# Kernel optimization log

Measured on AMD Instinct MI355X. Metric: run time of the kernel, lower is better.

The kernel has to match this reference:

```python
import jax
import jax.numpy as jnp
import numpy as np
from jax import lax

# Butterworth order-2 lowpass, Wn=0.25 (scipy.signal.butter(2, 0.25))
_B = [0.0976310729378175, 0.195262145875635, 0.0976310729378175]
_A = [1.0, -0.9428090415820634, 0.33333333333333337]


def setup_inputs() -> dict:
    key = jax.random.key(0)
    x = jax.random.normal(key, (128, 8, 32768), dtype=jnp.float32)
    b = jnp.array(_B, dtype=jnp.float32)
    a = jnp.array(_A, dtype=jnp.float32)
    return {"x": x, "b": b, "a": a}


def _odd_ext(x, n):
    # scipy-style odd extension along the last axis
    left = 2.0 * x[..., :1] - x[..., 1:n + 1][..., ::-1]
    right = 2.0 * x[..., -1:] - x[..., -n - 1:-1][..., ::-1]
    return jnp.concatenate([left, x, right], axis=-1)


def _lfilter(b, a, x):
    # Direct-form II transposed IIR filter along last axis, zero initial state.
    b = b / a[0]
    a = a / a[0]
    order = b.shape[0] - 1  # static
    b_tail, a_tail = b[1:], a[1:]
    z0 = jnp.zeros(x.shape[:-1] + (order,), dtype=x.dtype)
    xT = jnp.moveaxis(x, -1, 0)  # [T, ...batch]

    def step(z, xt):
        yt = b[0] * xt + z[..., 0]
        z_shift = jnp.concatenate([z[..., 1:], jnp.zeros_like(z[..., :1])], axis=-1)
        z_new = z_shift + b_tail * xt[..., None] - a_tail * yt[..., None]
        return z_new, yt

    _, yT = lax.scan(step, z0, xT)
    return jnp.moveaxis(yT, 0, -1)


def _filtfilt(x, a, b):
    y = _lfilter(b, a, x)
    y = _lfilter(b, a, y[..., ::-1])
    return y[..., ::-1]


def reference(x, b, a):
    scale = jnp.max(jnp.abs(x), axis=-1, keepdims=True)
    xn = x / scale
    padlen = 3 * max(int(a.shape[0]), int(b.shape[0]))  # static = 9
    xe = _odd_ext(xn, padlen)
    y = _filtfilt(xe, a, b)
    y = y[..., padlen:-padlen]
    return y * scale
```

## Files before the change

### kernel.cpp

```cpp
#include <hip/hip_runtime.h>


#define N_COLS 32768
#define PAD 9
#define LTOT  (N_COLS + 2 * PAD)
#define OUTEND (N_COLS + PAD)
#define WF 16
#define WB 16
#define CF 19
#define CB 17
#define LANES 64
#define P   (CB * LANES)
#define NSEG 31
#define SLOT (WF + CF * LANES)
#define WPB 4
#define TPB 256

__launch_bounds__(TPB, 4)
__global__ void filtfilt_kernel(const float* __restrict__ x,
                                const float* __restrict__ bco,
                                const float* __restrict__ aco,
                                float* __restrict__ out,
                                int rows) {
    __shared__ float xs_all[WPB][SLOT];
    const int tid = threadIdx.x;
    const int wid = tid >> 6;
    const int lane = tid & 63;
    float* __restrict__ xs = xs_all[wid];

    const int W = blockIdx.x * WPB + wid;
    const int row = W / NSEG;
    const int seg = W - row * NSEG;
    if (row >= rows) return;

    const float inv_a0 = 1.0f / aco[0];
    const float B0 = bco[0] * inv_a0;
    const float B1 = bco[1] * inv_a0;
    const float B2 = bco[2] * inv_a0;
    const float A1 = aco[1] * inv_a0;
    const float A2 = aco[2] * inv_a0;

    const int G = PAD + seg * P;
    const int A = G - WF;
    const float* __restrict__ xrow = x + (size_t)row * N_COLS;

    {
        const int g0 = (A - PAD > 0) ? (A - PAD) : 0;
        int g1 = G + CF * LANES; if (g1 > OUTEND) g1 = OUTEND; g1 -= PAD;
        const int off0 = g0 + PAD - A;
        const float4* __restrict__ xg4 = (const float4*)(xrow + g0);
        float4* __restrict__ s4 = (float4*)(xs + off0);
        const int nvec = (g1 - g0) >> 2;
        for (int i = lane; i < nvec; i += LANES) s4[i] = xg4[i];
    }
    if (seg == 0) {
        if (lane < WF) {
            const int t = lane - (WF - PAD);
            xs[lane] = (t >= 0) ? (2.0f * xrow[0] - xrow[PAD - t]) : 0.0f;
        }
    }
    if (seg == NSEG - 1) {
        const float x_last = xrow[N_COLS - 1];
        for (int o = (OUTEND - A) + lane; o < SLOT; o += LANES) {
            const int t = A + o;
            xs[o] = (t < LTOT) ? (2.0f * x_last - xrow[2 * N_COLS + PAD - 2 - t])
                               : 0.0f;
        }
    }

    const int f_off = CF * lane;
    float v[WF + CF];
#pragma unroll
    for (int k = 0; k < WF + CF; ++k) v[k] = xs[f_off + k];
    {
        float z0 = 0.0f, z1 = 0.0f;
#pragma unroll
        for (int k = 0; k < WF + CF; ++k) {
            const float xv = v[k];
            const float y = fmaf(B0, xv, z0);
            z0 = fmaf(-A1, y, fmaf(B1, xv, z1));
            z1 = fmaf(B2, xv, -A2 * y);
            v[k] = y;
        }
    }
#pragma unroll
    for (int k = WF; k < WF + CF; ++k) xs[f_off + k] = v[k];

    if (seg == NSEG - 1) {
        for (int o = (LTOT - A) + lane; o < SLOT; o += LANES) xs[o] = 0.0f;
    }

    const int b_off = CB * lane + WF;
    float w[CB + WB];
#pragma unroll
    for (int k = 0; k < CB + WB; ++k) w[k] = xs[b_off + k];
    {
        float z0 = 0.0f, z1 = 0.0f;
#pragma unroll
        for (int k = CB + WB - 1; k >= 0; --k) {
            const float xv = w[k];
            const float y = fmaf(B0, xv, z0);
            z0 = fmaf(-A1, y, fmaf(B1, xv, z1));
            z1 = fmaf(B2, xv, -A2 * y);
            if (k < CB) w[k] = y;
        }
    }
#pragma unroll
    for (int k = 0; k < CB; ++k) xs[b_off + k] = w[k];

    int nout = OUTEND - G; if (nout > P) nout = P;
    float* __restrict__ orow = out + (size_t)row * N_COLS + (G - PAD);
    const float4* __restrict__ s4 = (const float4*)(xs + WF);
    float4* __restrict__ o4 = (float4*)orow;
    const int nv = nout >> 2;
    for (int i = lane; i < nv; i += LANES) o4[i] = s4[i];
}

extern "C" void kernel_launch(void* const* d_in, const int* in_sizes, int n_in,
                              void* d_out, int out_size, void* d_ws, size_t ws_size,
                              hipStream_t stream) {
    const float* x = (const float*)d_in[0];
    const float* b = (const float*)d_in[1];
    const float* a = (const float*)d_in[2];
    float* out = (float*)d_out;
    const int rows = out_size / N_COLS;
    const int total_waves = rows * NSEG;
    const int blocks = (total_waves + WPB - 1) / WPB;
    filtfilt_kernel<<<blocks, TPB, 0, stream>>>(x, b, a, out, rows);
}
```

Before: 239.5 us.

## Unify forward/backward chunk size and keep forward results in registers for backward pass

Measured after the change: 237.9 us. No clear change (-0.7%).

```diff
diff --git a/kernel.cpp b/kernel.cpp
--- a/kernel.cpp
+++ b/kernel.cpp
@@ -7,14 +7,16 @@
 #define OUTEND (N_COLS + PAD)
 #define WF 16
 #define WB 16
-#define CF 19
-#define CB 17
+#define C  20
 #define LANES 64
-#define P   (CB * LANES)
-#define NSEG 31
-#define SLOT (WF + CF * LANES)
-#define WPB 4
-#define TPB 256
+#define P   (C * LANES)
+#define NSEG 26
+#define SLOT (WF + P + WB)
+#define WPB 2
+#define TPB 128
+
+#define LDS_PHASE_FENCE() do { asm volatile("" ::: "memory"); \
+                               __builtin_amdgcn_sched_barrier(0); } while (0)
 
 __launch_bounds__(TPB, 4)
 __global__ void filtfilt_kernel(const float* __restrict__ x,
@@ -46,7 +48,7 @@
 
     {
         const int g0 = (A - PAD > 0) ? (A - PAD) : 0;
-        int g1 = G + CF * LANES; if (g1 > OUTEND) g1 = OUTEND; g1 -= PAD;
+        int g1 = A + SLOT; if (g1 > OUTEND) g1 = OUTEND; g1 -= PAD;
         const int off0 = g0 + PAD - A;
         const float4* __restrict__ xg4 = (const float4*)(xrow + g0);
         float4* __restrict__ s4 = (float4*)(xs + off0);
@@ -68,52 +70,81 @@
         }
     }
 
-    const int f_off = CF * lane;
-    float v[WF + CF];
+    LDS_PHASE_FENCE();
+
+    const int f_off = C * lane;
+    float v[WF + C] __attribute__((aligned(16)));
 #pragma unroll
-    for (int k = 0; k < WF + CF; ++k) v[k] = xs[f_off + k];
-    {
-        float z0 = 0.0f, z1 = 0.0f;
+    for (int k = 0; k < (WF + C) / 4; ++k)
+        *(float4*)(v + 4 * k) = *(const float4*)(xs + f_off + 4 * k);
+    float fz0 = 0.0f, fz1 = 0.0f;
 #pragma unroll
-        for (int k = 0; k < WF + CF; ++k) {
-            const float xv = v[k];
-            const float y = fmaf(B0, xv, z0);
-            z0 = fmaf(-A1, y, fmaf(B1, xv, z1));
-            z1 = fmaf(B2, xv, -A2 * y);
-            v[k] = y;
-        }
+    for (int k = 0; k < WF + C; ++k) {
+        const float xv = v[k];
+        const float y = fmaf(B0, xv, fz0);
+        fz0 = fmaf(-A1, y, fmaf(B1, xv, fz1));
+        fz1 = fmaf(B2, xv, -A2 * y);
+        v[k] = y;
     }
 #pragma unroll
-    for (int k = WF; k < WF + CF; ++k) xs[f_off + k] = v[k];
+    for (int k = 0; k < WB / 4; ++k)
+        *(float4*)(xs + f_off + WF + 4 * k) = *(const float4*)(v + WF + 4 * k);
+
+    if (lane == LANES - 1) {
+        float e[WB] __attribute__((aligned(16)));
+#pragma unroll
+        for (int k = 0; k < WB / 4; ++k)
+            *(float4*)(e + 4 * k) = *(const float4*)(xs + WF + P + 4 * k);
+#pragma unroll
+        for (int k = 0; k < WB; ++k) {
+            const float xv = e[k];
+            const float y = fmaf(B0, xv, fz0);
+            fz0 = fmaf(-A1, y, fmaf(B1, xv, fz1));
+            fz1 = fmaf(B2, xv, -A2 * y);
+            e[k] = y;
+        }
+#pragma unroll
+        for (int k = 0; k < WB / 4; ++k)
+            *(float4*)(xs + WF + P + 4 * k) = *(const float4*)(e + 4 * k);
+    }
 
     if (seg == NSEG - 1) {
         for (int o = (LTOT - A) + lane; o < SLOT; o += LANES) xs[o] = 0.0f;
     }
 
-    const int b_off = CB * lane + WF;
-    float w[CB + WB];
+    LDS_PHASE_FENCE();
+
+    const int b0 = C * lane;
+    float r[WB] __attribute__((aligned(16)));
 #pragma unroll
-    for (int k = 0; k < CB + WB; ++k) w[k] = xs[b_off + k];
-    {
-        float z0 = 0.0f, z1 = 0.0f;
+    for (int k = 0; k < WB / 4; ++k)
+        *(float4*)(r + 4 * k) = *(const float4*)(xs + b0 + WF + C + 4 * k);
+    if (seg == NSEG - 1) {
+        const int LIM = LTOT - G;
 #pragma unroll
-        for (int k = CB + WB - 1; k >= 0; --k) {
-            const float xv = w[k];
-            const float y = fmaf(B0, xv, z0);
-            z0 = fmaf(-A1, y, fmaf(B1, xv, z1));
-            z1 = fmaf(B2, xv, -A2 * y);
-            if (k < CB) w[k] = y;
-        }
+        for (int k = 0; k < C; ++k) if (b0 + k >= LIM) v[WF + k] = 0.0f;
+    }
+    float bz0 = 0.0f, bz1 = 0.0f;
+#pragma unroll
+    for (int k = C + WB - 1; k >= 0; --k) {
+        const float xv = (k < C) ? v[WF + k] : r[k - C];
+        const float y = fmaf(B0, xv, bz0);
+        bz0 = fmaf(-A1, y, fmaf(B1, xv, bz1));
+        bz1 = fmaf(B2, xv, -A2 * y);
+        if (k < C) v[WF + k] = y;
     }
 #pragma unroll
-    for (int k = 0; k < CB; ++k) xs[b_off + k] = w[k];
+    for (int k = 0; k < C / 4; ++k)
+        *(float4*)(xs + b0 + WF + 4 * k) = *(const float4*)(v + WF + 4 * k);
+
+    LDS_PHASE_FENCE();
 
     int nout = OUTEND - G; if (nout > P) nout = P;
     float* __restrict__ orow = out + (size_t)row * N_COLS + (G - PAD);
-    const float4* __restrict__ s4 = (const float4*)(xs + WF);
+    const float4* __restrict__ s4o = (const float4*)(xs + WF);
     float4* __restrict__ o4 = (float4*)orow;
     const int nv = nout >> 2;
-    for (int i = lane; i < nv; i += LANES) o4[i] = s4[i];
+    for (int i = lane; i < nv; i += LANES) o4[i] = s4o[i];
 }
 
 extern "C" void kernel_launch(void* const* d_in, const int* in_sizes, int n_in,
```

## Load filter windows directly from global memory into registers, dropping shared staging

Applied to the files above, without the earlier changes.

Measured after the change: 252.4 us. 1.05x slower.

```diff
diff --git a/kernel.cpp b/kernel.cpp
--- a/kernel.cpp
+++ b/kernel.cpp
@@ -4,15 +4,14 @@
 #define N_COLS 32768
 #define PAD 9
 #define LTOT  (N_COLS + 2 * PAD)
-#define OUTEND (N_COLS + PAD)
 #define WF 16
 #define WB 16
-#define CF 19
-#define CB 17
+#define C  32
 #define LANES 64
-#define P   (CB * LANES)
-#define NSEG 31
-#define SLOT (WF + CF * LANES)
+#define P   (C * LANES)
+#define NSEG (N_COLS / P)
+#define WIN (WF + C + WB)
+#define NLD (WIN / 4)
 #define WPB 4
 #define TPB 256
 
@@ -22,15 +21,12 @@
                                 const float* __restrict__ aco,
                                 float* __restrict__ out,
                                 int rows) {
-    __shared__ float xs_all[WPB][SLOT];
     const int tid = threadIdx.x;
     const int wid = tid >> 6;
     const int lane = tid & 63;
-    float* __restrict__ xs = xs_all[wid];
-
     const int W = blockIdx.x * WPB + wid;
-    const int row = W / NSEG;
-    const int seg = W - row * NSEG;
+    const int row = W >> 4;
+    const int seg = W & (NSEG - 1);
     if (row >= rows) return;
 
     const float inv_a0 = 1.0f / aco[0];
@@ -40,80 +36,68 @@
     const float A1 = aco[1] * inv_a0;
     const float A2 = aco[2] * inv_a0;
 
-    const int G = PAD + seg * P;
-    const int A = G - WF;
     const float* __restrict__ xrow = x + (size_t)row * N_COLS;
+    const int xbase = seg * P + C * lane - WF;
 
-    {
-        const int g0 = (A - PAD > 0) ? (A - PAD) : 0;
-        int g1 = G + CF * LANES; if (g1 > OUTEND) g1 = OUTEND; g1 -= PAD;
-        const int off0 = g0 + PAD - A;
-        const float4* __restrict__ xg4 = (const float4*)(xrow + g0);
-        float4* __restrict__ s4 = (float4*)(xs + off0);
-        const int nvec = (g1 - g0) >> 2;
-        for (int i = lane; i < nvec; i += LANES) s4[i] = xg4[i];
+    float v[WIN];
+#pragma unroll
+    for (int j = 0; j < NLD; ++j) {
+        int idx = xbase + 4 * j;
+        idx = (idx < 0) ? 0 : idx;
+        idx = (idx > N_COLS - 4) ? (N_COLS - 4) : idx;
+        *(float4*)(v + 4 * j) = *(const float4*)(xrow + idx);
     }
-    if (seg == 0) {
-        if (lane < WF) {
-            const int t = lane - (WF - PAD);
-            xs[lane] = (t >= 0) ? (2.0f * xrow[0] - xrow[PAD - t]) : 0.0f;
+
+    if (seg == 0 && lane == 0) {
+        const float x0 = xrow[0];
+#pragma unroll
+        for (int k = 0; k < WF; ++k) {
+            const int t = k - (WF - PAD);
+            v[k] = (t < 0) ? 0.0f : (2.0f * x0 - xrow[PAD - t]);
         }
     }
-    if (seg == NSEG - 1) {
-        const float x_last = xrow[N_COLS - 1];
-        for (int o = (OUTEND - A) + lane; o < SLOT; o += LANES) {
-            const int t = A + o;
-            xs[o] = (t < LTOT) ? (2.0f * x_last - xrow[2 * N_COLS + PAD - 2 - t])
-                               : 0.0f;
-        }
+    if (seg == NSEG - 1 && lane == LANES - 1) {
+        const float xl = xrow[N_COLS - 1];
+#pragma unroll
+        for (int k = 48; k < 57; ++k)
+            v[k] = 2.0f * xl - xrow[32814 - k];
+#pragma unroll
+        for (int k = 57; k < WIN; ++k) v[k] = 0.0f;
     }
 
-    const int f_off = CF * lane;
-    float v[WF + CF];
-#pragma unroll
-    for (int k = 0; k < WF + CF; ++k) v[k] = xs[f_off + k];
     {
         float z0 = 0.0f, z1 = 0.0f;
 #pragma unroll
-        for (int k = 0; k < WF + CF; ++k) {
+        for (int k = 0; k < WIN; ++k) {
             const float xv = v[k];
             const float y = fmaf(B0, xv, z0);
             z0 = fmaf(-A1, y, fmaf(B1, xv, z1));
             z1 = fmaf(B2, xv, -A2 * y);
-            v[k] = y;
+            if (k >= WF) v[k] = y;
         }
     }
+
+    if (seg == NSEG - 1 && lane == LANES - 1) {
 #pragma unroll
-    for (int k = WF; k < WF + CF; ++k) xs[f_off + k] = v[k];
-
-    if (seg == NSEG - 1) {
-        for (int o = (LTOT - A) + lane; o < SLOT; o += LANES) xs[o] = 0.0f;
+        for (int k = 57; k < WIN; ++k) v[k] = 0.0f;
     }
 
-    const int b_off = CB * lane + WF;
-    float w[CB + WB];
-#pragma unroll
-    for (int k = 0; k < CB + WB; ++k) w[k] = xs[b_off + k];
     {
         float z0 = 0.0f, z1 = 0.0f;
 #pragma unroll
-        for (int k = CB + WB - 1; k >= 0; --k) {
-            const float xv = w[k];
+        for (int k = WIN - 1; k >= WF; --k) {
+            const float xv = v[k];
             const float y = fmaf(B0, xv, z0);
             z0 = fmaf(-A1, y, fmaf(B1, xv, z1));
             z1 = fmaf(B2, xv, -A2 * y);
-            if (k < CB) w[k] = y;
+            if (k < WF + C) v[k] = y;
         }
     }
+
+    float* __restrict__ orow = out + (size_t)row * N_COLS + (xbase + WF);
 #pragma unroll
-    for (int k = 0; k < CB; ++k) xs[b_off + k] = w[k];
-
-    int nout = OUTEND - G; if (nout > P) nout = P;
-    float* __restrict__ orow = out + (size_t)row * N_COLS + (G - PAD);
-    const float4* __restrict__ s4 = (const float4*)(xs + WF);
-    float4* __restrict__ o4 = (float4*)orow;
-    const int nv = nout >> 2;
-    for (int i = lane; i < nv; i += LANES) o4[i] = s4[i];
+    for (int j = 0; j < C / 4; ++j)
+        *(float4*)(orow + 4 * j) = *(const float4*)(v + WF + 4 * j);
 }
 
 extern "C" void kernel_launch(void* const* d_in, const int* in_sizes, int n_in,
```
